# Kernel tuning notes

Hardware: AMD Instinct MI355X
Metric: run time of the kernel (lower is better)

Reference implementation:

```python
import jax, jax.numpy as jnp
import numpy as np

B, N, C, H = 16, 577, 768, 12
D = C // H
BETA = 1.0
KEEP_RATIO = 0.5


def setup_inputs() -> dict:
    key = jax.random.key(0)
    k0, k1, k2, k3 = jax.random.split(key, 4)
    x = jax.random.normal(k0, (B, N, C), dtype=jnp.float32)
    # UCB visit-count buffer, strictly positive as accumulated counts would be
    ucb_count_score = jax.random.uniform(k1, (H, N), dtype=jnp.float32) * 50.0 + 1.0
    Wqkv = jax.random.normal(k2, (3 * C, C), dtype=jnp.float32) * 0.02
    Wproj = jax.random.normal(k3, (C, C), dtype=jnp.float32) * 0.02
    bproj = jnp.zeros((C,), dtype=jnp.float32)
    counter = 60  # > 50 so pruning path is taken
    return {"x": x, "ucb_count_score": ucb_count_score, "Wqkv": Wqkv,
            "Wproj": Wproj, "bproj": bproj, "counter": counter}


def reference(x, ucb_count_score, Wqkv, Wproj, bproj, counter):
    # UCBAttention.forward with pruning_enabled=True, selection_mode='ucb',
    # ucb_update_enabled=True, exclude_cls=True, dropout=0 (eval).
    Bs, Ns, Cs = x.shape
    scale = D ** -0.5
    k_keep = max(1, int((Ns - 1) * KEEP_RATIO))  # _get_k with keep_ratio

    qkv = (x @ Wqkv.T).reshape(Bs, Ns, 3, H, D).transpose(2, 0, 3, 1, 4)  # [3,B,H,N,D]
    q, k, v = qkv[0], qkv[1], qkv[2]
    attn_scores = jnp.einsum('bhqd,bhkd->bhqk', q, k) * scale
    attn_probs = jax.nn.softmax(attn_scores, axis=-1)  # [B,H,N,N]

    # UCB scores over patches (CLS excluded)
    patch_scores = attn_probs[:, :, :, 1:].mean(axis=2)            # [B,H,N-1]
    expl = BETA * jnp.sqrt(jnp.log(counter + 1.0) / (ucb_count_score[:, 1:] + 1e-6))
    ucb_scores = patch_scores + expl[None, :, :]                   # [B,H,N-1]
    global_ucb = ucb_scores.mean(axis=1)                           # [B,N-1]
    _, topk_rel = jax.lax.top_k(global_ucb, k_keep)                # [B,k]
    kept = topk_rel + 1                                            # token indices

    # keep-vector: CLS (0) always kept; mask[i,j] = kept[i] OR kept[j]
    kv_mask = (jnp.zeros((Bs, Ns), attn_probs.dtype)
               .at[jnp.arange(Bs)[:, None], kept].set(1.0)
               .at[:, 0].set(1.0))                                 # [B,N]
    mask = jnp.maximum(kv_mask[:, None, :, None], kv_mask[:, None, None, :])  # [B,1,N,N]

    pruned = attn_probs * mask
    pruned = pruned / (pruned.sum(axis=-1, keepdims=True) + 1e-8)
    context = jnp.einsum('bhqk,bhkd->bhqd', pruned, v)             # [B,H,N,D]

    out = context.transpose(0, 2, 1, 3).reshape(Bs, Ns, Cs) @ Wproj.T + bproj

    # score_delta: +1/B at each kept token column, broadcast over heads
    delta = jnp.zeros((Ns,), jnp.float32).at[kept.reshape(-1)].add(1.0 / Bs)
    score_delta = jnp.broadcast_to(delta[None, :], ucb_count_score.shape)
    return out, score_delta, kept
```

## Files before the change

### kernel.cpp

```cpp
#include <hip/hip_runtime.h>
#include <cstdio>
#include <cstdint>

#define B_    16
#define N_    577
#define C_    768
#define H_    12
#define D_    64
#define KKEEP 288
#define SCALE 0.125f
#define LOG2E 1.4426950408889634f
#define M_TOT (B_ * N_)
#define NKT   24
#define PLROW ((size_t)N_ * 64)

typedef __bf16 bf16x8_t __attribute__((ext_vector_type(8)));
typedef __bf16 bf16x4_t __attribute__((ext_vector_type(4)));
typedef float  f32x4_t  __attribute__((ext_vector_type(4)));
typedef unsigned int u32x4_t __attribute__((ext_vector_type(4)));
typedef unsigned int u32x2_t __attribute__((ext_vector_type(2)));

__device__ __forceinline__ f32x4_t mfma_bf16(bf16x8_t a, bf16x8_t b, f32x4_t c) {
    return __builtin_amdgcn_mfma_f32_16x16x32_bf16(a, b, c, 0, 0, 0);
}

__device__ __forceinline__ void gload16(const ushort* g, ushort* l) {
    __builtin_amdgcn_global_load_lds(
        (const __attribute__((address_space(1))) void*)g,
        (__attribute__((address_space(3))) void*)l, 16, 0, 0);
}
#define VMCNT(n) asm volatile("s_waitcnt vmcnt(" #n ")" ::: "memory")
#define LGKM0()  asm volatile("s_waitcnt lgkmcnt(0)" ::: "memory")
#define SB() __builtin_amdgcn_sched_barrier(0)

__device__ __forceinline__ int xcd_swz(int bid, int nwg) {
    int q = nwg >> 3, r = nwg & 7;
    int xcd = bid & 7, off = bid >> 3;
    int base = (xcd < r) ? xcd * (q + 1) : r * (q + 1) + (xcd - r) * q;
    return base + off;
}

__device__ __forceinline__ void splitf(float x, unsigned int &hi, unsigned int &lo) {
    unsigned int u = __float_as_uint(x);
    hi = u >> 16;
    float r = x - __uint_as_float(u & 0xffff0000u);
    lo = __float_as_uint(r) >> 16;
}
__device__ __forceinline__ unsigned int bf16rne(float x) {
    unsigned int u = __float_as_uint(x);
    return (u + 0x7fffu + ((u >> 16) & 1u)) >> 16;
}

__device__ __forceinline__ void pack_tile(const float* __restrict__ src,
                                          ushort* __restrict__ dH,
                                          ushort* __restrict__ dL,
                                          int nrows, int tile) {
    int kt = tile % NKT, mt = tile / NKT;
    int w = threadIdx.x;
    int row = w >> 1, h = w & 1;
    int m = mt * 128 + row;
    int sw = (row >> 1) & 3;
    float f[16];
    if (m < nrows) {
        const float* s = src + (size_t)m * C_ + kt * 32;
        int sa = (2 * h) ^ sw, sb = (2 * h + 1) ^ sw;
        *(float4*)&f[0]  = *(const float4*)(s + sa * 8);
        *(float4*)&f[4]  = *(const float4*)(s + sa * 8 + 4);
        *(float4*)&f[8]  = *(const float4*)(s + sb * 8);
        *(float4*)&f[12] = *(const float4*)(s + sb * 8 + 4);
    } else {
#pragma unroll
        for (int i = 0; i < 16; i++) f[i] = 0.f;
    }
    unsigned hi[16], lo[16];
#pragma unroll
    for (int i = 0; i < 16; i++) splitf(f[i], hi[i], lo[i]);
    u32x4_t h0 = {hi[0] | (hi[1] << 16), hi[2] | (hi[3] << 16),
                  hi[4] | (hi[5] << 16), hi[6] | (hi[7] << 16)};
    u32x4_t h1 = {hi[8] | (hi[9] << 16), hi[10] | (hi[11] << 16),
                  hi[12] | (hi[13] << 16), hi[14] | (hi[15] << 16)};
    u32x4_t l0 = {lo[0] | (lo[1] << 16), lo[2] | (lo[3] << 16),
                  lo[4] | (lo[5] << 16), lo[6] | (lo[7] << 16)};
    u32x4_t l1 = {lo[8] | (lo[9] << 16), lo[10] | (lo[11] << 16),
                  lo[12] | (lo[13] << 16), lo[14] | (lo[15] << 16)};
    size_t dbase = (size_t)tile * 4096 + row * 32;
    *(u32x4_t*)&dH[dbase + (2 * h) * 8]     = h0;
    *(u32x4_t*)&dH[dbase + (2 * h + 1) * 8] = h1;
    *(u32x4_t*)&dL[dbase + (2 * h) * 8]     = l0;
    *(u32x4_t*)&dL[dbase + (2 * h + 1) * 8] = l1;
}

#define NXP 1752
#define NWP 432
#define NRNE 288
#define NZ  37

__global__ __launch_bounds__(256) void pack_all_kernel(const float* __restrict__ x,
                                                       const float* __restrict__ Wqkv,
                                                       const float* __restrict__ Wproj,
                                                       ushort* __restrict__ XplH,
                                                       ushort* __restrict__ XplL,
                                                       ushort* __restrict__ WplH,
                                                       ushort* __restrict__ WplL,
                                                       ushort* __restrict__ Wpjb,
                                                       float* __restrict__ kvmask) {
    int bid = blockIdx.x;
    if (bid < NXP) {
        pack_tile(x, XplH, XplL, M_TOT, bid);
    } else if (bid < NXP + NWP) {
        pack_tile(Wqkv, WplH, WplL, 3 * C_, bid - NXP);
    } else if (bid < NXP + NWP + NRNE) {
        int i = (bid - NXP - NWP) * 256 + threadIdx.x;
        float4 f0 = ((const float4*)Wproj)[2 * i];
        float4 f1 = ((const float4*)Wproj)[2 * i + 1];
        u32x4_t o = {bf16rne(f0.x) | (bf16rne(f0.y) << 16),
                     bf16rne(f0.z) | (bf16rne(f0.w) << 16),
                     bf16rne(f1.x) | (bf16rne(f1.y) << 16),
                     bf16rne(f1.z) | (bf16rne(f1.w) << 16)};
        *(u32x4_t*)&Wpjb[(size_t)i * 8] = o;
    } else {
        int i = (bid - NXP - NWP - NRNE) * 256 + threadIdx.x;
        if (i < B_ * N_) kvmask[i] = 0.f;
    }
}

__device__ __forceinline__ bf16x8_t fragT(const ushort* H, int row, int c, int ls) {
    int phys = ((c << 2) + ls) ^ (row & 7);
    return __builtin_bit_cast(bf16x8_t, *(const u32x4_t*)&H[(row << 6) + (phys << 3)]);
}

__global__ __launch_bounds__(256) void gemm_qkv_mfma(const ushort* __restrict__ XplH,
                                                     const ushort* __restrict__ XplL,
                                                     const ushort* __restrict__ WplH,
                                                     const ushort* __restrict__ WplL,
                                                     ushort* __restrict__ qhp,
                                                     ushort* __restrict__ qlp,
                                                     ushort* __restrict__ khp,
                                                     ushort* __restrict__ klp,
                                                     ushort* __restrict__ vtp) {
    __shared__ ushort SMEM[32768];
    ushort* Ah = SMEM;
    ushort* Al = SMEM + 8192;
    ushort* Bh = SMEM + 16384;
    ushort* Bl = SMEM + 24576;
    const int bid = xcd_swz(blockIdx.x, 18 * 73);
    const int bx = bid % 18, by = bid / 18;
    const int tid = threadIdx.x;
    const int lane = tid & 63, wave = tid >> 6;
    const int wr = wave >> 1, wc = wave & 1;
    const int lr = lane & 15, ls = lane >> 4;
    const int m0 = by * 128;
    const int o0 = wave * 1024, o1 = o0 + 512;
    const int la = lane * 8;
    const size_t abase = (size_t)by * NKT * 4096;
    const size_t bbase = (size_t)bx * NKT * 4096;
    f32x4_t acc[4][4] = {};

    if (bx < 12) {
        auto stage = [&](int buf, int kt) {
            const size_t ta = abase + (size_t)kt * 4096;
            const size_t tb = bbase + (size_t)kt * 4096;
            gload16(XplH + ta + o0 + la, &Ah[buf * 4096 + o0]);
            gload16(XplH + ta + o1 + la, &Ah[buf * 4096 + o1]);
            gload16(XplL + ta + o0 + la, &Al[buf * 4096 + o0]);
            gload16(XplL + ta + o1 + la, &Al[buf * 4096 + o1]);
            gload16(WplH + tb + o0 + la, &Bh[buf * 4096 + o0]);
            gload16(WplH + tb + o1 + la, &Bh[buf * 4096 + o1]);
            gload16(WplL + tb + o0 + la, &Bl[buf * 4096 + o0]);
            gload16(WplL + tb + o1 + la, &Bl[buf * 4096 + o1]);
        };
        stage(0, 0);
#pragma unroll 1
        for (int kt = 0; kt < NKT; ++kt) {
            const int cur = kt & 1;
            if (kt + 1 < NKT) {
                stage(cur ^ 1, kt + 1);
                VMCNT(8);
            } else {
                VMCNT(0);
            }
            SB();
            __builtin_amdgcn_s_barrier();
            SB();
            bf16x8_t fah[4], fal[4], fbh[4], fbl[4];
#pragma unroll
            for (int i = 0; i < 4; i++) {
                int rowA = wr * 64 + i * 16 + lr;
                int pa = ls ^ ((rowA >> 1) & 3);
                fah[i] = __builtin_bit_cast(bf16x8_t, *(const u32x4_t*)&Ah[cur * 4096 + rowA * 32 + pa * 8]);
                fal[i] = __builtin_bit_cast(bf16x8_t, *(const u32x4_t*)&Al[cur * 4096 + rowA * 32 + pa * 8]);
                int rowB = wc * 64 + i * 16 + lr;
                int pb = ls ^ ((rowB >> 1) & 3);
                fbh[i] = __builtin_bit_cast(bf16x8_t, *(const u32x4_t*)&Bh[cur * 4096 + rowB * 32 + pb * 8]);
                fbl[i] = __builtin_bit_cast(bf16x8_t, *(const u32x4_t*)&Bl[cur * 4096 + rowB * 32 + pb * 8]);
            }
#pragma unroll
            for (int i = 0; i < 4; i++)
#pragma unroll
                for (int j = 0; j < 4; j++) {
                    acc[i][j] = mfma_bf16(fah[i], fbh[j], acc[i][j]);
                    acc[i][j] = mfma_bf16(fah[i], fbl[j], acc[i][j]);
                    acc[i][j] = mfma_bf16(fal[i], fbh[j], acc[i][j]);
                }
            if (kt + 1 < NKT) {
                SB();
                __builtin_amdgcn_s_barrier();
            }
        }
        const int n0 = bx * 128;
        const int s = n0 / C_;
        __syncthreads();
        unsigned* T = (unsigned*)SMEM;
        const float sc = (s == 0) ? SCALE * LOG2E : 1.0f;
#pragma unroll
        for (int j = 0; j < 4; j++) {
            int nl = wc * 64 + j * 16 + lr;
#pragma unroll
            for (int i = 0; i < 4; i++) {
#pragma unroll
                for (int r = 0; r < 4; r++) {
                    int ml = wr * 64 + i * 16 + ls * 4 + r;
                    unsigned hi, lo;
                    splitf(acc[i][j][r] * sc, hi, lo);
                    int idx = ml * 128 + ((((nl >> 3) ^ ((ml >> 2) & 7)) << 3) | (nl & 7));
                    T[idx] = hi | (lo << 16);
                }
            }
        }
        __syncthreads();
        ushort* dh = (s == 1) ? khp : qhp;
        ushort* dl = (s == 1) ? klp : qlp;
        const int hh0 = (n0 % C_) / D_;
#pragma unroll
        for (int it = 0; it < 8; ++it) {
            int g = it * 256 + tid;
            int sl = g & 7;
            int m_local = (g >> 3) & 127;
            int hh_half = g >> 10;
            int m = m0 + m_local;
            if (m < M_TOT) {
                int b = m / N_, n = m % N_;
                int dg = sl ^ (n & 7);
                int grp = (hh_half * 8 + dg) ^ ((m_local >> 2) & 7);
                const unsigned* src = &T[m_local * 128 + grp * 8];
                u32x4_t a = *(const u32x4_t*)src;
                u32x4_t bvv = *(const u32x4_t*)(src + 4);
                u32x4_t hiv = {(a[0] & 0xffffu) | (a[1] << 16),
                               (a[2] & 0xffffu) | (a[3] << 16),
                               (bvv[0] & 0xffffu) | (bvv[1] << 16),
                               (bvv[2] & 0xffffu) | (bvv[3] << 16)};
                u32x4_t lov = {(a[0] >> 16) | (a[1] & 0xffff0000u),
                               (a[2] >> 16) | (a[3] & 0xffff0000u),
                               (bvv[0] >> 16) | (bvv[1] & 0xffff0000u),
                               (bvv[2] >> 16) | (bvv[3] & 0xffff0000u)};
                size_t off = (size_t)(b * H_ + hh0 + hh_half) * PLROW + (size_t)n * 64 + sl * 8;
                *(u32x4_t*)&dh[off] = hiv;
                *(u32x4_t*)&dl[off] = lov;
            }
        }
    } else {
        auto stage = [&](int buf, int kt) {
            const size_t ta = abase + (size_t)kt * 4096;
            const size_t tb = bbase + (size_t)kt * 4096;
            gload16(XplH + ta + o0 + la, &Ah[buf * 4096 + o0]);
            gload16(XplH + ta + o1 + la, &Ah[buf * 4096 + o1]);
            gload16(XplL + ta + o0 + la, &Al[buf * 4096 + o0]);
            gload16(XplL + ta + o1 + la, &Al[buf * 4096 + o1]);
            gload16(WplH + tb + o0 + la, &Bh[buf * 4096 + o0]);
            gload16(WplH + tb + o1 + la, &Bh[buf * 4096 + o1]);
        };
        stage(0, 0);
#pragma unroll 1
        for (int kt = 0; kt < NKT; ++kt) {
            const int cur = kt & 1;
            if (kt + 1 < NKT) {
                stage(cur ^ 1, kt + 1);
                VMCNT(6);
            } else {
                VMCNT(0);
            }
            SB();
            __builtin_amdgcn_s_barrier();
            SB();
            bf16x8_t fah[4], fal[4], fbh[4];
#pragma unroll
            for (int i = 0; i < 4; i++) {
                int rowA = wr * 64 + i * 16 + lr;
                int pa = ls ^ ((rowA >> 1) & 3);
                fah[i] = __builtin_bit_cast(bf16x8_t, *(const u32x4_t*)&Ah[cur * 4096 + rowA * 32 + pa * 8]);
                fal[i] = __builtin_bit_cast(bf16x8_t, *(const u32x4_t*)&Al[cur * 4096 + rowA * 32 + pa * 8]);
                int rowB = wc * 64 + i * 16 + lr;
                int pb = ls ^ ((rowB >> 1) & 3);
                fbh[i] = __builtin_bit_cast(bf16x8_t, *(const u32x4_t*)&Bh[cur * 4096 + rowB * 32 + pb * 8]);
            }
#pragma unroll
            for (int i = 0; i < 4; i++)
#pragma unroll
                for (int j = 0; j < 4; j++) {
                    acc[i][j] = mfma_bf16(fah[i], fbh[j], acc[i][j]);
                    acc[i][j] = mfma_bf16(fal[i], fbh[j], acc[i][j]);
                }
            if (kt + 1 < NKT) {
                SB();
                __builtin_amdgcn_s_barrier();
            }
        }
        const int n0v = (bx - 12) * 128;
#pragma unroll
        for (int j = 0; j < 4; j++) {
            int ng = n0v + wc * 64 + j * 16 + lr;
            int hh = ng / D_;
            int d = ng % D_;
#pragma unroll
            for (int i = 0; i < 4; i++) {
                int mg0 = m0 + wr * 64 + i * 16 + ls * 4;
#pragma unroll
                for (int r = 0; r < 4; r++) {
                    int m = mg0 + r;
                    if (m < M_TOT) {
                        int b = m / N_, n = m % N_;
                        int jt = n >> 6, jl = n & 63;
                        size_t off = ((size_t)(b * H_ + hh) * 10 + jt) * 4096 +
                                     (size_t)d * 64 + (((jl >> 3) ^ (d & 7)) << 3) + (jl & 7);
                        vtp[off] = __builtin_bit_cast(unsigned short, (__bf16)acc[i][j][r]);
                    }
                }
            }
        }
    }
}

__global__ __launch_bounds__(512) void attn_rowsum_mfma(const ushort* __restrict__ qh,
                                                        const ushort* __restrict__ ql,
                                                        const ushort* __restrict__ kh,
                                                        const ushort* __restrict__ kl,
                                                        float* __restrict__ w) {
    __shared__ ushort Qh[8192], Ql[8192];
    __shared__ ushort Kh[4096], Kl[4096];
    __shared__ float red[8][64];
    const int bid = xcd_swz(blockIdx.x, 5 * B_ * H_);
    const int bh = bid / 5, q0 = (bid % 5) * 128;
    const int tid = threadIdx.x, lane = tid & 63, wv = tid >> 6;
    const int wg = wv >> 2, wl = wv & 3;
    const int lr = lane & 15, ls = lane >> 4;
    const size_t bho = (size_t)bh * PLROW;
    const ushort* qhp = qh + bho; const ushort* qlp = ql + bho;
    const ushort* khp = kh + bho; const ushort* klp = kl + bho;
    auto qrow = [&](int rr) { return (size_t)min(q0 + wv * 16 + rr * 8 + (lane >> 3), N_ - 1) * 64 + (lane & 7) * 8; };
    gload16(qhp + qrow(0), &Qh[wv * 1024]);
    gload16(qhp + qrow(1), &Qh[wv * 1024 + 512]);
    gload16(qlp + qrow(0), &Ql[wv * 1024]);
    gload16(qlp + qrow(1), &Ql[wv * 1024 + 512]);
    auto krow = [&](int j0) { return (size_t)min(j0 + wv * 8 + (lane >> 3), N_ - 1) * 64 + (lane & 7) * 8; };
    auto stageK = [&](int j0) {
        gload16(khp + krow(j0), &Kh[wv * 512]);
        gload16(klp + krow(j0), &Kl[wv * 512]);
    };
    stageK(0);
    VMCNT(0);
    __syncthreads();
    bf16x8_t fqh[4][2], fql[4][2];
#pragma unroll
    for (int i = 0; i < 4; i++)
#pragma unroll
        for (int c = 0; c < 2; c++) {
            fqh[i][c] = fragT(Qh, wg * 64 + i * 16 + lr, c, ls);
            fql[i][c] = fragT(Ql, wg * 64 + i * 16 + lr, c, ls);
        }
    float rs[4] = {0.f, 0.f, 0.f, 0.f};
#pragma unroll 1
    for (int t = 0; t < 10; ++t) {
        bf16x8_t fkh[2], fkl[2];
#pragma unroll
        for (int c = 0; c < 2; c++) {
            fkh[c] = fragT(Kh, wl * 16 + lr, c, ls);
            fkl[c] = fragT(Kl, wl * 16 + lr, c, ls);
        }
        int jbase = t * 64 + wl * 16 + ls * 4;
#pragma unroll
        for (int i = 0; i < 4; i++) {
            f32x4_t s = {0.f, 0.f, 0.f, 0.f};
            __builtin_amdgcn_s_setprio(1);
#pragma unroll
            for (int c = 0; c < 2; c++) {
                s = mfma_bf16(fkh[c], fqh[i][c], s);
                s = mfma_bf16(fkh[c], fql[i][c], s);
                s = mfma_bf16(fkl[c], fqh[i][c], s);
            }
            __builtin_amdgcn_s_setprio(0);
#pragma unroll
            for (int r = 0; r < 4; r++)
                rs[i] += (jbase + r < N_) ? __builtin_amdgcn_exp2f(s[r]) : 0.f;
        }
        if (t < 9) {
            SB(); __builtin_amdgcn_s_barrier(); SB();
            stageK((t + 1) * 64);
            VMCNT(0);
            SB(); __builtin_amdgcn_s_barrier(); SB();
        }
    }
#pragma unroll
    for (int i = 0; i < 4; i++) {
        float v2 = rs[i];
        v2 += __shfl_xor(v2, 16);
        v2 += __shfl_xor(v2, 32);
        if (ls == 0) red[wv][i * 16 + lr] = v2;
    }
    __syncthreads();
    if (tid < 128) {
        int grp = tid >> 6, qlc = tid & 63;
        float s = red[grp * 4 + 0][qlc] + red[grp * 4 + 1][qlc] +
                  red[grp * 4 + 2][qlc] + red[grp * 4 + 3][qlc];
        int qn = q0 + tid;
        if (qn < N_) w[(size_t)bh * N_ + qn] = 1.0f / s;
    }
}

__global__ __launch_bounds__(512) void attn_colsum_mfma(const ushort* __restrict__ qh,
                                                        const ushort* __restrict__ ql,
                                                        const ushort* __restrict__ kh,
                                                        const ushort* __restrict__ kl,
                                                        const float* __restrict__ w,
                                                        float* __restrict__ colsum) {
    __shared__ ushort KhS[8192], KlS[8192];
    __shared__ ushort Qh[4096], Ql[4096];
    __shared__ float wsAll[640];
    __shared__ float red[8][64];
    const int bid = xcd_swz(blockIdx.x, 5 * B_ * H_);
    const int bh = bid / 5, j0 = (bid % 5) * 128;
    const int tid = threadIdx.x, lane = tid & 63, wv = tid >> 6;
    const int wg = wv >> 2, wl = wv & 3;
    const int lr = lane & 15, ls = lane >> 4;
    const size_t bho = (size_t)bh * PLROW;
    const ushort* qhp = qh + bho; const ushort* qlp = ql + bho;
    const ushort* khp = kh + bho; const ushort* klp = kl + bho;
    auto krow = [&](int rr) { return (size_t)min(j0 + wv * 16 + rr * 8 + (lane >> 3), N_ - 1) * 64 + (lane & 7) * 8; };
    gload16(khp + krow(0), &KhS[wv * 1024]);
    gload16(khp + krow(1), &KhS[wv * 1024 + 512]);
    gload16(klp + krow(0), &KlS[wv * 1024]);
    gload16(klp + krow(1), &KlS[wv * 1024 + 512]);
    auto qrow2 = [&](int qt) { return (size_t)min(qt + wv * 8 + (lane >> 3), N_ - 1) * 64 + (lane & 7) * 8; };
    auto stageQ = [&](int qt) {
        gload16(qhp + qrow2(qt), &Qh[wv * 512]);
        gload16(qlp + qrow2(qt), &Ql[wv * 512]);
    };
    stageQ(0);
    for (int i2 = tid; i2 < 640; i2 += 512)
        wsAll[i2] = (i2 < N_) ? w[(size_t)bh * N_ + i2] : 0.f;
    VMCNT(0);
    __syncthreads();
    bf16x8_t fkh[4][2], fkl[4][2];
#pragma unroll
    for (int i = 0; i < 4; i++)
#pragma unroll
        for (int c = 0; c < 2; c++) {
            fkh[i][c] = fragT(KhS, wg * 64 + i * 16 + lr, c, ls);
            fkl[i][c] = fragT(KlS, wg * 64 + i * 16 + lr, c, ls);
        }
    float cs[4] = {0.f, 0.f, 0.f, 0.f};
#pragma unroll 1
    for (int t = 0; t < 10; ++t) {
        bf16x8_t fqh[2], fql[2];
#pragma unroll
        for (int c = 0; c < 2; c++) {
            fqh[c] = fragT(Qh, wl * 16 + lr, c, ls);
            fql[c] = fragT(Ql, wl * 16 + lr, c, ls);
        }
        float wq[4];
#pragma unroll
        for (int r = 0; r < 4; r++) wq[r] = wsAll[t * 64 + wl * 16 + ls * 4 + r];
#pragma unroll
        for (int i = 0; i < 4; i++) {
            f32x4_t s = {0.f, 0.f, 0.f, 0.f};
            __builtin_amdgcn_s_setprio(1);
#pragma unroll
            for (int c = 0; c < 2; c++) {
                s = mfma_bf16(fqh[c], fkh[i][c], s);
                s = mfma_bf16(fql[c], fkh[i][c], s);
                s = mfma_bf16(fqh[c], fkl[i][c], s);
            }
            __builtin_amdgcn_s_setprio(0);
#pragma unroll
            for (int r = 0; r < 4; r++) cs[i] += __builtin_amdgcn_exp2f(s[r]) * wq[r];
        }
        if (t < 9) {
            SB(); __builtin_amdgcn_s_barrier(); SB();
            stageQ((t + 1) * 64);
            VMCNT(0);
            SB(); __builtin_amdgcn_s_barrier(); SB();
        }
    }
#pragma unroll
    for (int i = 0; i < 4; i++) {
        float v2 = cs[i];
        v2 += __shfl_xor(v2, 16);
        v2 += __shfl_xor(v2, 32);
        if (ls == 0) red[wv][i * 16 + lr] = v2;
    }
    __syncthreads();
    if (tid < 128) {
        int grp = tid >> 6, jlc = tid & 63;
        float t2 = red[grp * 4 + 0][jlc] + red[grp * 4 + 1][jlc] +
                   red[grp * 4 + 2][jlc] + red[grp * 4 + 3][jlc];
        int jn = j0 + tid;
        if (jn < N_) colsum[(size_t)bh * N_ + jn] = t2;
    }
}

__global__ __launch_bounds__(512) void topk_kernel(const float* __restrict__ colsum,
                                                   const float* __restrict__ ucb_count,
                                                   const int* __restrict__ counter,
                                                   float* __restrict__ kept_out,
                                                   float* __restrict__ kvmask) {
    __shared__ float sv[1024];
    __shared__ int si[1024];
    int b = blockIdx.x, tid = threadIdx.x;
    float lc = logf((float)counter[0] + 1.0f);
    for (int t = tid; t < 1024; t += 512) {
        if (t < N_ - 1) {
            int tok = t + 1;
            float accv = 0.f;
#pragma unroll
            for (int h = 0; h < H_; h++) {
                float csv = colsum[(size_t)(b * H_ + h) * N_ + tok];
                float patch = csv * (1.0f / (float)N_);
                float cnt = ucb_count[h * N_ + tok];
                float expl = sqrtf(lc / (cnt + 1e-6f));
                accv += patch + expl;
            }
            sv[t] = accv * (1.0f / (float)H_);
            si[t] = t;
        } else {
            sv[t] = -INFINITY;
            si[t] = 1 << 20;
        }
    }
    __syncthreads();
    for (int kk = 2; kk <= 1024; kk <<= 1) {
        for (int jj = kk >> 1; jj > 0; jj >>= 1) {
            for (int t = tid; t < 1024; t += 512) {
                int ixj = t ^ jj;
                if (ixj > t) {
                    float v1 = sv[t], v2 = sv[ixj];
                    int i1 = si[t], i2 = si[ixj];
                    bool before21 = (v2 > v1) || (v2 == v1 && i2 < i1);
                    bool dirDesc = ((t & kk) == 0);
                    if (before21 == dirDesc) {
                        sv[t] = v2; sv[ixj] = v1;
                        si[t] = i2; si[ixj] = i1;
                    }
                }
            }
            __syncthreads();
        }
    }
    for (int r = tid; r < KKEEP; r += 512) {
        int tok = si[r] + 1;
        kept_out[b * KKEEP + r] = (float)tok;
        kvmask[b * N_ + tok] = 1.0f;
    }
    if (tid == 0) kvmask[b * N_] = 1.0f;
}

__global__ __launch_bounds__(512) void attn_ctx_mfma(const ushort* __restrict__ qh,
                                                     const ushort* __restrict__ ql,
                                                     const ushort* __restrict__ kh,
                                                     const ushort* __restrict__ vtp,
                                                     const float* __restrict__ kvmask,
                                                     ushort* __restrict__ ctxb,
                                                     float* __restrict__ sd) {
    if (blockIdx.x >= 5 * B_ * H_) {
        int idx = (blockIdx.x - 5 * B_ * H_) * 512 + threadIdx.x;
        if (idx < H_ * N_) {
            int n = idx % N_;
            float d = 0.f;
            if (n != 0) {
#pragma unroll
                for (int b = 0; b < B_; b++) d += kvmask[b * N_ + n];
            }
            sd[idx] = d * (1.0f / (float)B_);
        }
        return;
    }
    __shared__ ushort Kh[2][4096], Vt[2][4096];
    __shared__ ushort Pl[2][4096];
    __shared__ float mkAll[640];
    float (*red)[64] = (float(*)[64])&Pl[0][0];
    float* inv = (float*)&Pl[1][0];
    const int bid = xcd_swz(blockIdx.x, 5 * B_ * H_);
    const int bh = bid / 5, q0 = (bid % 5) * 128;
    const int b = bh / H_, h = bh % H_;
    const int tid = threadIdx.x, lane = tid & 63, wv = tid >> 6;
    const int wg = wv >> 2, wl = wv & 3;
    const int lr = lane & 15, ls = lane >> 4;
    const size_t bho = (size_t)bh * PLROW;
    const ushort* qhp = qh + bho; const ushort* qlp = ql + bho;
    const ushort* khp = kh + bho;
    const ushort* vtb = vtp + (size_t)bh * 10 * 4096;
    ushort* PlS = &Pl[0][0];
    for (int i2 = tid; i2 < 640; i2 += 512)
        mkAll[i2] = (i2 < N_) ? kvmask[(size_t)b * N_ + i2] : 0.f;
    auto qrow = [&](int rr) { return (size_t)min(q0 + wv * 16 + rr * 8 + (lane >> 3), N_ - 1) * 64 + (lane & 7) * 8; };
    bf16x8_t fqh[4][2], fql[4][2];
    gload16(qhp + qrow(0), &PlS[wv * 1024]);
    gload16(qhp + qrow(1), &PlS[wv * 1024 + 512]);
    VMCNT(0); __syncthreads();
#pragma unroll
    for (int i = 0; i < 4; i++)
#pragma unroll
        for (int c = 0; c < 2; c++)
            fqh[i][c] = fragT(PlS, wg * 64 + i * 16 + lr, c, ls);
    __syncthreads();
    gload16(qlp + qrow(0), &PlS[wv * 1024]);
    gload16(qlp + qrow(1), &PlS[wv * 1024 + 512]);
    VMCNT(0); __syncthreads();
#pragma unroll
    for (int i = 0; i < 4; i++)
#pragma unroll
        for (int c = 0; c < 2; c++)
            fql[i][c] = fragT(PlS, wg * 64 + i * 16 + lr, c, ls);
    __syncthreads();
    auto krow = [&](int j0) { return (size_t)min(j0 + wv * 8 + (lane >> 3), N_ - 1) * 64 + (lane & 7) * 8; };
    auto stageKV = [&](int buf, int t) {
        gload16(khp + krow(t * 64), &Kh[buf][wv * 512]);
        gload16(vtb + (size_t)t * 4096 + wv * 512 + lane * 8, &Vt[buf][wv * 512]);
    };
    float mq[4];
#pragma unroll
    for (int i = 0; i < 4; i++) mq[i] = mkAll[q0 + wg * 64 + i * 16 + lr];
    stageKV(0, 0);
    f32x4_t acc[4] = {};
    float psums[4] = {0.f, 0.f, 0.f, 0.f};
#pragma unroll 1
    for (int t = 0; t < 10; ++t) {
        const int cur = t & 1;
        if (t < 9) { stageKV(cur ^ 1, t + 1); VMCNT(2); }
        else      { VMCNT(0); }
        SB(); __builtin_amdgcn_s_barrier(); SB();
        bf16x8_t fkh[2];
#pragma unroll
        for (int c = 0; c < 2; c++)
            fkh[c] = fragT(Kh[cur], wl * 16 + lr, c, ls);
        int jloc = wl * 16 + ls * 4;
        float jmv[4], jbias[4];
#pragma unroll
        for (int r = 0; r < 4; r++) {
            int j = t * 64 + jloc + r;
            jmv[r] = mkAll[t * 64 + jloc + r];
            jbias[r] = (j < N_) ? 0.f : -16384.f;
        }
#pragma unroll
        for (int i = 0; i < 4; i++) {
            f32x4_t s = {0.f, 0.f, 0.f, 0.f};
            __builtin_amdgcn_s_setprio(1);
#pragma unroll
            for (int c = 0; c < 2; c++) {
                s = mfma_bf16(fkh[c], fqh[i][c], s);
                s = mfma_bf16(fkh[c], fql[i][c], s);
            }
            __builtin_amdgcn_s_setprio(0);
            bf16x4_t pb;
            float mqi = mq[i];
#pragma unroll
            for (int r = 0; r < 4; r++) {
                float p = __builtin_amdgcn_exp2f(s[r] + jbias[r]) * fmaxf(mqi, jmv[r]);
                psums[i] += p;
                pb[r] = (__bf16)p;
            }
            int row = i * 16 + lr;
            int slot = ((wl << 1) + (ls >> 1)) ^ (row & 7);
            *(u32x2_t*)&Pl[wg][(row << 6) + (slot << 3) + ((ls & 1) << 2)] =
                __builtin_bit_cast(u32x2_t, pb);
        }
        SB(); LGKM0(); SB();
        __builtin_amdgcn_s_barrier();
        SB();
        bf16x8_t fv[2];
#pragma unroll
        for (int c = 0; c < 2; c++) fv[c] = fragT(Vt[cur], wl * 16 + lr, c, ls);
        __builtin_amdgcn_s_setprio(1);
#pragma unroll
        for (int i = 0; i < 4; i++) {
            bf16x8_t fp0 = fragT(Pl[wg], i * 16 + lr, 0, ls);
            bf16x8_t fp1 = fragT(Pl[wg], i * 16 + lr, 1, ls);
            acc[i] = mfma_bf16(fv[0], fp0, acc[i]);
            acc[i] = mfma_bf16(fv[1], fp1, acc[i]);
        }
        __builtin_amdgcn_s_setprio(0);
        if (t < 9) { SB(); __builtin_amdgcn_s_barrier(); }
    }
    __syncthreads();
#pragma unroll
    for (int i = 0; i < 4; i++) {
        float v2 = psums[i];
        v2 += __shfl_xor(v2, 16);
        v2 += __shfl_xor(v2, 32);
        if (ls == 0) red[wv][i * 16 + lr] = v2;
    }
    __syncthreads();
    if (tid < 128) {
        int grp = tid >> 6, qlc = tid & 63;
        float t2 = red[grp * 4 + 0][qlc] + red[grp * 4 + 1][qlc] +
                   red[grp * 4 + 2][qlc] + red[grp * 4 + 3][qlc];
        inv[tid] = 1.0f / (t2 + 1e-8f);
    }
    __syncthreads();
#pragma unroll
    for (int i = 0; i < 4; i++) {
        int qn = q0 + wg * 64 + i * 16 + lr;
        if (qn < N_) {
            float rn = inv[wg * 64 + i * 16 + lr];
            bf16x4_t ov;
            ov[0] = (__bf16)(acc[i][0] * rn);
            ov[1] = (__bf16)(acc[i][1] * rn);
            ov[2] = (__bf16)(acc[i][2] * rn);
            ov[3] = (__bf16)(acc[i][3] * rn);
            *(u32x2_t*)&ctxb[((size_t)(b * N_ + qn)) * C_ + h * D_ + wl * 16 + ls * 4] =
                __builtin_bit_cast(u32x2_t, ov);
        }
    }
}

__global__ __launch_bounds__(256) void gemm_proj_mfma(const ushort* __restrict__ Actx,
                                                      const ushort* __restrict__ Wb,
                                                      const float* __restrict__ bias,
                                                      float* __restrict__ out) {
    __shared__ ushort Ab[128 * 32], Bb[128 * 32];
    const int bid = xcd_swz(blockIdx.x, 6 * 73);
    const int bx = bid % 6, by = bid / 6;
    const int tid = threadIdx.x;
    const int lane = tid & 63, wave = tid >> 6;
    const int wr = wave >> 1, wc = wave & 1;
    const int lr = lane & 15, ls = lane >> 4;
    const int m0 = by * 128, n0 = bx * 128;
    const int srow = tid >> 1, shalf = tid & 1;
    const int arow = min(m0 + srow, M_TOT - 1);
    const ushort* aptr = Actx + (size_t)arow * C_ + shalf * 16;
    const ushort* bptr = Wb + (size_t)(n0 + srow) * C_ + shalf * 16;
    const int swz = (srow >> 1) & 3;
    const int sidx = srow * 32;
    const int p0 = (shalf * 2 + 0) ^ swz, p1 = (shalf * 2 + 1) ^ swz;
    f32x4_t acc[4][4] = {};
#pragma unroll 1
    for (int k0 = 0; k0 < C_; k0 += 32) {
        __syncthreads();
        {
            u32x4_t c0 = *(const u32x4_t*)(aptr + k0);
            u32x4_t c1 = *(const u32x4_t*)(aptr + k0 + 8);
            *(u32x4_t*)&Ab[sidx + p0 * 8] = c0;
            *(u32x4_t*)&Ab[sidx + p1 * 8] = c1;
        }
        {
            u32x4_t c0 = *(const u32x4_t*)(bptr + k0);
            u32x4_t c1 = *(const u32x4_t*)(bptr + k0 + 8);
            *(u32x4_t*)&Bb[sidx + p0 * 8] = c0;
            *(u32x4_t*)&Bb[sidx + p1 * 8] = c1;
        }
        __syncthreads();
        bf16x8_t fa[4], fb[4];
#pragma unroll
        for (int i = 0; i < 4; i++) {
            int rowA = wr * 64 + i * 16 + lr;
            int pa = ls ^ ((rowA >> 1) & 3);
            fa[i] = __builtin_bit_cast(bf16x8_t, *(const u32x4_t*)&Ab[rowA * 32 + pa * 8]);
            int rowB = wc * 64 + i * 16 + lr;
            int pb = ls ^ ((rowB >> 1) & 3);
            fb[i] = __builtin_bit_cast(bf16x8_t, *(const u32x4_t*)&Bb[rowB * 32 + pb * 8]);
        }
#pragma unroll
        for (int i = 0; i < 4; i++)
#pragma unroll
            for (int j = 0; j < 4; j++)
                acc[i][j] = mfma_bf16(fa[i], fb[j], acc[i][j]);
    }
#pragma unroll
    for (int j = 0; j < 4; j++) {
        int ng = n0 + wc * 64 + j * 16 + lr;
        float bb = bias[ng];
#pragma unroll
        for (int i = 0; i < 4; i++) {
            int mg0 = m0 + wr * 64 + i * 16 + ls * 4;
#pragma unroll
            for (int r = 0; r < 4; r++) {
                int m = mg0 + r;
                if (m < M_TOT) out[(size_t)m * C_ + ng] = acc[i][j][r] + bb;
            }
        }
    }
}

extern "C" void kernel_launch(void* const* d_in, const int* in_sizes, int n_in,
                              void* d_out, int out_size, void* d_ws, size_t ws_size,
                              hipStream_t stream) {
    const float* x     = (const float*)d_in[0];
    const float* ucb   = (const float*)d_in[1];
    const float* Wqkv  = (const float*)d_in[2];
    const float* Wproj = (const float*)d_in[3];
    const float* bproj = (const float*)d_in[4];
    const int*   counter = (const int*)d_in[5];

    const size_t BHN  = (size_t)B_ * H_ * N_;
    const size_t XPL  = (size_t)(73 * 128) * C_;
    const size_t WPL  = (size_t)3 * C_ * C_;
    const size_t WPJ  = (size_t)C_ * C_;
    const size_t PLN  = (size_t)192 * PLROW;
    const size_t VTSZ = (size_t)192 * 10 * 4096;

    ushort* qhp  = (ushort*)d_ws;
    ushort* qlp  = qhp + PLN;
    ushort* khp  = qlp + PLN;
    ushort* klp  = khp + PLN;
    ushort* vtp  = klp + PLN;
    ushort* XplH = vtp + VTSZ;
    ushort* XplL = XplH + XPL;
    ushort* ctxb = XplH;
    ushort* WplH = XplL + XPL;
    ushort* WplL = WplH + WPL;
    ushort* Wpjb = WplL + WPL;
    float*  w    = (float*)(Wpjb + WPJ);
    float*  colsum = w + BHN;
    float*  kvmask = colsum + BHN;
    size_t need = ((char*)(kvmask + (size_t)B_ * N_)) - (char*)d_ws;
    if (ws_size < need) {
        fprintf(stderr, "kernel_launch: ws too small, need %zu have %zu\n",
                need, ws_size);
        return;
    }

    float* out  = (float*)d_out;
    float* sd   = out + (size_t)B_ * N_ * C_;
    float* kept = sd + (size_t)H_ * N_;

    pack_all_kernel<<<NXP + NWP + NRNE + NZ, 256, 0, stream>>>(
        x, Wqkv, Wproj, XplH, XplL, WplH, WplL, Wpjb, kvmask);

    gemm_qkv_mfma<<<18 * 73, 256, 0, stream>>>(XplH, XplL, WplH, WplL,
                                               qhp, qlp, khp, klp, vtp);
    attn_rowsum_mfma<<<5 * B_ * H_, 512, 0, stream>>>(qhp, qlp, khp, klp, w);
    attn_colsum_mfma<<<5 * B_ * H_, 512, 0, stream>>>(qhp, qlp, khp, klp, w, colsum);
    topk_kernel<<<B_, 512, 0, stream>>>(colsum, ucb, counter, kept, kvmask);
    attn_ctx_mfma<<<5 * B_ * H_ + 14, 512, 0, stream>>>(qhp, qlp, khp, vtp,
                                                        kvmask, ctxb, sd);
    gemm_proj_mfma<<<6 * 73, 256, 0, stream>>>(ctxb, Wpjb, bproj, out);
}
```

Baseline: 289.6 us.

## Pre-tile proj GEMM operands and double-buffer with async LDS loads; overlap K/Q staging

The context tensor and Wproj are now written directly in a swizzled 128x32 tile layout, so the projection GEMM can stream whole tiles into double-buffered LDS with direct global-to-LDS loads. This replaces the synchronous load-then-sync loop. The rowsum and colsum attention kernels now issue the next K/Q stage right after fragments are read, overlapping it with the MFMA work and dropping one barrier per iteration. The risk is that the scattered tiled stores in the ctx kernel are less coalesced, and the tile index math has to be correct for the padded last M tile.

```diff
diff --git a/kernel.cpp b/kernel.cpp
--- a/kernel.cpp
+++ b/kernel.cpp
@@ -90,9 +90,41 @@
     *(u32x4_t*)&dL[dbase + (2 * h + 1) * 8] = l1;
 }
 
+__device__ __forceinline__ void pack_tile_rne(const float* __restrict__ src,
+                                              ushort* __restrict__ dst,
+                                              int nrows, int tile) {
+    int kt = tile % NKT, mt = tile / NKT;
+    int w = threadIdx.x;
+    int row = w >> 1, h = w & 1;
+    int m = mt * 128 + row;
+    int sw = (row >> 1) & 3;
+    float f[16];
+    if (m < nrows) {
+        const float* s = src + (size_t)m * C_ + kt * 32;
+        int sa = (2 * h) ^ sw, sb = (2 * h + 1) ^ sw;
+        *(float4*)&f[0]  = *(const float4*)(s + sa * 8);
+        *(float4*)&f[4]  = *(const float4*)(s + sa * 8 + 4);
+        *(float4*)&f[8]  = *(const float4*)(s + sb * 8);
+        *(float4*)&f[12] = *(const float4*)(s + sb * 8 + 4);
+    } else {
+#pragma unroll
+        for (int i = 0; i < 16; i++) f[i] = 0.f;
+    }
+    unsigned hi[16];
+#pragma unroll
+    for (int i = 0; i < 16; i++) hi[i] = bf16rne(f[i]);
+    u32x4_t h0 = {hi[0] | (hi[1] << 16), hi[2] | (hi[3] << 16),
+                  hi[4] | (hi[5] << 16), hi[6] | (hi[7] << 16)};
+    u32x4_t h1 = {hi[8] | (hi[9] << 16), hi[10] | (hi[11] << 16),
+                  hi[12] | (hi[13] << 16), hi[14] | (hi[15] << 16)};
+    size_t dbase = (size_t)tile * 4096 + row * 32;
+    *(u32x4_t*)&dst[dbase + (2 * h) * 8]     = h0;
+    *(u32x4_t*)&dst[dbase + (2 * h + 1) * 8] = h1;
+}
+
 #define NXP 1752
 #define NWP 432
-#define NRNE 288
+#define NPJ 144
 #define NZ  37
 
 __global__ __launch_bounds__(256) void pack_all_kernel(const float* __restrict__ x,
@@ -109,17 +141,10 @@
         pack_tile(x, XplH, XplL, M_TOT, bid);
     } else if (bid < NXP + NWP) {
         pack_tile(Wqkv, WplH, WplL, 3 * C_, bid - NXP);
-    } else if (bid < NXP + NWP + NRNE) {
-        int i = (bid - NXP - NWP) * 256 + threadIdx.x;
-        float4 f0 = ((const float4*)Wproj)[2 * i];
-        float4 f1 = ((const float4*)Wproj)[2 * i + 1];
-        u32x4_t o = {bf16rne(f0.x) | (bf16rne(f0.y) << 16),
-                     bf16rne(f0.z) | (bf16rne(f0.w) << 16),
-                     bf16rne(f1.x) | (bf16rne(f1.y) << 16),
-                     bf16rne(f1.z) | (bf16rne(f1.w) << 16)};
-        *(u32x4_t*)&Wpjb[(size_t)i * 8] = o;
+    } else if (bid < NXP + NWP + NPJ) {
+        pack_tile_rne(Wproj, Wpjb, C_, bid - NXP - NWP);
     } else {
-        int i = (bid - NXP - NWP - NRNE) * 256 + threadIdx.x;
+        int i = (bid - NXP - NWP - NPJ) * 256 + threadIdx.x;
         if (i < B_ * N_) kvmask[i] = 0.f;
     }
 }
@@ -376,6 +401,10 @@
             fkh[c] = fragT(Kh, wl * 16 + lr, c, ls);
             fkl[c] = fragT(Kl, wl * 16 + lr, c, ls);
         }
+        LGKM0(); SB();
+        __builtin_amdgcn_s_barrier();
+        SB();
+        if (t < 9) stageK((t + 1) * 64);
         int jbase = t * 64 + wl * 16 + ls * 4;
 #pragma unroll
         for (int i = 0; i < 4; i++) {
@@ -393,10 +422,9 @@
                 rs[i] += (jbase + r < N_) ? __builtin_amdgcn_exp2f(s[r]) : 0.f;
         }
         if (t < 9) {
-            SB(); __builtin_amdgcn_s_barrier(); SB();
-            stageK((t + 1) * 64);
-            VMCNT(0);
-            SB(); __builtin_amdgcn_s_barrier(); SB();
+            VMCNT(0); SB();
+            __builtin_amdgcn_s_barrier();
+            SB();
         }
     }
 #pragma unroll
@@ -469,6 +497,10 @@
         float wq[4];
 #pragma unroll
         for (int r = 0; r < 4; r++) wq[r] = wsAll[t * 64 + wl * 16 + ls * 4 + r];
+        LGKM0(); SB();
+        __builtin_amdgcn_s_barrier();
+        SB();
+        if (t < 9) stageQ((t + 1) * 64);
 #pragma unroll
         for (int i = 0; i < 4; i++) {
             f32x4_t s = {0.f, 0.f, 0.f, 0.f};
@@ -484,10 +516,9 @@
             for (int r = 0; r < 4; r++) cs[i] += __builtin_amdgcn_exp2f(s[r]) * wq[r];
         }
         if (t < 9) {
-            SB(); __builtin_amdgcn_s_barrier(); SB();
-            stageQ((t + 1) * 64);
-            VMCNT(0);
-            SB(); __builtin_amdgcn_s_barrier(); SB();
+            VMCNT(0); SB();
+            __builtin_amdgcn_s_barrier();
+            SB();
         }
     }
 #pragma unroll
@@ -715,17 +746,22 @@
             ov[1] = (__bf16)(acc[i][1] * rn);
             ov[2] = (__bf16)(acc[i][2] * rn);
             ov[3] = (__bf16)(acc[i][3] * rn);
-            *(u32x2_t*)&ctxb[((size_t)(b * N_ + qn)) * C_ + h * D_ + wl * 16 + ls * 4] =
-                __builtin_bit_cast(u32x2_t, ov);
-        }
-    }
-}
-
-__global__ __launch_bounds__(256) void gemm_proj_mfma(const ushort* __restrict__ Actx,
-                                                      const ushort* __restrict__ Wb,
+            int m = b * N_ + qn;
+            int col = h * D_ + wl * 16 + ls * 4;
+            int mt = m >> 7, rowl = m & 127;
+            int kt2 = col >> 5, c32 = col & 31;
+            int phys = (c32 >> 3) ^ ((rowl >> 1) & 3);
+            size_t off = ((size_t)(mt * NKT + kt2)) * 4096 + rowl * 32 + phys * 8 + (c32 & 7);
+            *(u32x2_t*)&ctxb[off] = __builtin_bit_cast(u32x2_t, ov);
+        }
+    }
+}
+
+__global__ __launch_bounds__(256) void gemm_proj_mfma(const ushort* __restrict__ Apl,
+                                                      const ushort* __restrict__ Bpl,
                                                       const float* __restrict__ bias,
                                                       float* __restrict__ out) {
-    __shared__ ushort Ab[128 * 32], Bb[128 * 32];
+    __shared__ ushort Ab[2][4096], Bb[2][4096];
     const int bid = xcd_swz(blockIdx.x, 6 * 73);
     const int bx = bid % 6, by = bid / 6;
     const int tid = threadIdx.x;
@@ -733,45 +769,52 @@
     const int wr = wave >> 1, wc = wave & 1;
     const int lr = lane & 15, ls = lane >> 4;
     const int m0 = by * 128, n0 = bx * 128;
-    const int srow = tid >> 1, shalf = tid & 1;
-    const int arow = min(m0 + srow, M_TOT - 1);
-    const ushort* aptr = Actx + (size_t)arow * C_ + shalf * 16;
-    const ushort* bptr = Wb + (size_t)(n0 + srow) * C_ + shalf * 16;
-    const int swz = (srow >> 1) & 3;
-    const int sidx = srow * 32;
-    const int p0 = (shalf * 2 + 0) ^ swz, p1 = (shalf * 2 + 1) ^ swz;
+    const int o0 = wave * 1024, o1 = o0 + 512;
+    const int la = lane * 8;
+    const size_t abase = (size_t)by * NKT * 4096;
+    const size_t bbase = (size_t)bx * NKT * 4096;
     f32x4_t acc[4][4] = {};
+
+    auto stage = [&](int buf, int kt) {
+        const size_t ta = abase + (size_t)kt * 4096;
+        const size_t tb = bbase + (size_t)kt * 4096;
+        gload16(Apl + ta + o0 + la, &Ab[buf][o0]);
+        gload16(Apl + ta + o1 + la, &Ab[buf][o1]);
+        gload16(Bpl + tb + o0 + la, &Bb[buf][o0]);
+        gload16(Bpl + tb + o1 + la, &Bb[buf][o1]);
+    };
+    stage(0, 0);
 #pragma unroll 1
-    for (int k0 = 0; k0 < C_; k0 += 32) {
-        __syncthreads();
-        {
-            u32x4_t c0 = *(const u32x4_t*)(aptr + k0);
-            u32x4_t c1 = *(const u32x4_t*)(aptr + k0 + 8);
-            *(u32x4_t*)&Ab[sidx + p0 * 8] = c0;
-            *(u32x4_t*)&Ab[sidx + p1 * 8] = c1;
-        }
-        {
-            u32x4_t c0 = *(const u32x4_t*)(bptr + k0);
-            u32x4_t c1 = *(const u32x4_t*)(bptr + k0 + 8);
-            *(u32x4_t*)&Bb[sidx + p0 * 8] = c0;
-            *(u32x4_t*)&Bb[sidx + p1 * 8] = c1;
-        }
-        __syncthreads();
+    for (int kt = 0; kt < NKT; ++kt) {
+        const int cur = kt & 1;
+        if (kt + 1 < NKT) {
+            stage(cur ^ 1, kt + 1);
+            VMCNT(4);
+        } else {
+            VMCNT(0);
+        }
+        SB();
+        __builtin_amdgcn_s_barrier();
+        SB();
         bf16x8_t fa[4], fb[4];
 #pragma unroll
         for (int i = 0; i < 4; i++) {
             int rowA = wr * 64 + i * 16 + lr;
             int pa = ls ^ ((rowA >> 1) & 3);
-            fa[i] = __builtin_bit_cast(bf16x8_t, *(const u32x4_t*)&Ab[rowA * 32 + pa * 8]);
+            fa[i] = __builtin_bit_cast(bf16x8_t, *(const u32x4_t*)&Ab[cur][rowA * 32 + pa * 8]);
             int rowB = wc * 64 + i * 16 + lr;
             int pb = ls ^ ((rowB >> 1) & 3);
-            fb[i] = __builtin_bit_cast(bf16x8_t, *(const u32x4_t*)&Bb[rowB * 32 + pb * 8]);
+            fb[i] = __builtin_bit_cast(bf16x8_t, *(const u32x4_t*)&Bb[cur][rowB * 32 + pb * 8]);
         }
 #pragma unroll
         for (int i = 0; i < 4; i++)
 #pragma unroll
             for (int j = 0; j < 4; j++)
                 acc[i][j] = mfma_bf16(fa[i], fb[j], acc[i][j]);
+        if (kt + 1 < NKT) {
+            SB();
+            __builtin_amdgcn_s_barrier();
+        }
     }
 #pragma unroll
     for (int j = 0; j < 4; j++) {
@@ -831,7 +874,7 @@
     float* sd   = out + (size_t)B_ * N_ * C_;
     float* kept = sd + (size_t)H_ * N_;
 
-    pack_all_kernel<<<NXP + NWP + NRNE + NZ, 256, 0, stream>>>(
+    pack_all_kernel<<<NXP + NWP + NPJ + NZ, 256, 0, stream>>>(
         x, Wqkv, Wproj, XplH, XplL, WplH, WplL, Wpjb, kvmask);
 
     gemm_qkv_mfma<<<18 * 73, 256, 0, stream>>>(XplH, XplL, WplH, WplL,
```

After: 282.6 us. 1.02x faster.
